# Kernel tuning notes

Hardware: AMD Instinct MI355X
Metric: run time of the kernel (lower is better)

## Reference

```python
import jax, jax.numpy as jnp
import numpy as np

N_NODES = 50000

def _gcn_layer(x, src, dst, W, b, n_nodes):
    # x: [N, F_in]; src/dst: [E+N] (self-loops already appended)
    h = x @ W  # [N, F_out]
    deg = jax.ops.segment_sum(jnp.ones_like(dst, dtype=h.dtype), dst, num_segments=n_nodes)
    dinv = jnp.where(deg > 0, jax.lax.rsqrt(deg), 0.0)  # deg^{-1/2}
    norm = dinv[src] * dinv[dst]  # [E+N]
    msg = h[src] * norm[:, None]  # gather + scale
    out = jax.ops.segment_sum(msg, dst, num_segments=n_nodes)  # scatter-add
    return out + b

def setup_inputs() -> dict:
    key = jax.random.key(0)
    k1, k2, k3, k4 = jax.random.split(key, 4)
    d = 128
    E = 800000
    x = jax.random.normal(k1, (N_NODES, d), dtype=jnp.float32)
    edge_index = jax.random.randint(k2, (2, E), 0, N_NODES, dtype=jnp.int64)
    W1 = jax.random.normal(k3, (d, d), dtype=jnp.float32) / np.sqrt(d)
    b1 = jnp.zeros((d,), dtype=jnp.float32)
    W2 = jax.random.normal(k4, (d, d), dtype=jnp.float32) / np.sqrt(d)
    b2 = jnp.zeros((d,), dtype=jnp.float32)
    return {"x": x, "edge_index": edge_index, "W1": W1, "b1": b1, "W2": W2, "b2": b2}

def reference(x, edge_index, W1, b1, W2, b2):
    n = x.shape[0]
    loops = jnp.arange(n, dtype=edge_index.dtype)
    src = jnp.concatenate([edge_index[0], loops])  # add self-loops
    dst = jnp.concatenate([edge_index[1], loops])
    h = _gcn_layer(x, src, dst, W1, b1, n)
    h = jax.nn.relu(h)
    z = _gcn_layer(h, src, dst, W2, b2, n)
    return z
```

## Files before the change

### kernel.cpp

```cpp
#include <hip/hip_runtime.h>
#include <hip/hip_fp16.h>

#define NF 128
#define NP 8192
#define KC 32

typedef _Float16 half8 __attribute__((ext_vector_type(8)));
typedef float    floatx4 __attribute__((ext_vector_type(4)));

__global__ __launch_bounds__(256) void prep_k(
    const float* __restrict__ W1, const float* __restrict__ W2,
    __half* __restrict__ WT1, __half* __restrict__ WT2)
{
    int idx = blockIdx.x * 256 + threadIdx.x;
    const float* W = (idx < 16384) ? W1 : W2;
    __half* WT     = (idx < 16384) ? WT1 : WT2;
    int j = idx & 16383;
    int nn = j & 127, k = j >> 7;
    WT[nn * NF + k] = __float2half(W[k * NF + nn]);
}

__global__ __launch_bounds__(512) void count2_k(
    const int* __restrict__ dst, int* __restrict__ pcnt, int E, int N, int Ec)
{
    __shared__ int lcnt[NP];
    const int p = blockIdx.x & 7, c = blockIdx.x >> 3;
    const int Np = (N + 7) >> 3;
    const int lo = p * Np, hi = min(lo + Np, N);
    const int sz = hi - lo;
    for (int i = threadIdx.x; i < sz; i += 512) lcnt[i] = 0;
    __syncthreads();

    const int e0 = c * Ec, e1 = min(e0 + Ec, E);
    for (int e = e0 + (int)threadIdx.x * 4; e + 3 < e1; e += 512 * 4) {
        int4 d = *(const int4*)(dst + e);
        if (d.x >= lo && d.x < hi) atomicAdd(&lcnt[d.x - lo], 1);
        if (d.y >= lo && d.y < hi) atomicAdd(&lcnt[d.y - lo], 1);
        if (d.z >= lo && d.z < hi) atomicAdd(&lcnt[d.z - lo], 1);
        if (d.w >= lo && d.w < hi) atomicAdd(&lcnt[d.w - lo], 1);
    }
    int rem0 = e0 + ((e1 - e0) & ~3);
    for (int e = rem0 + (int)threadIdx.x; e < e1; e += 512) {
        int d = dst[e];
        if (d >= lo && d < hi) atomicAdd(&lcnt[d - lo], 1);
    }
    __syncthreads();
    for (int i = threadIdx.x; i < sz; i += 512)
        pcnt[(size_t)c * N + lo + i] = lcnt[i];
}

__global__ __launch_bounds__(256) void pscan2_k(
    int* __restrict__ pcnt, float* __restrict__ dinv,
    int* __restrict__ rowptr, int* __restrict__ blocksum, int n, int N)
{
    __shared__ int sm[256];
    int tid = threadIdx.x;
    int bin = blockIdx.x * 256 + tid;
    int total = 0;
    if (bin < n) {
        #pragma unroll 4
        for (int c = 0; c < KC; c++) {
            size_t o = (size_t)c * N + bin;
            int v = pcnt[o];
            pcnt[o] = total;
            total += v;
        }
        dinv[bin] = rsqrtf((float)total + 1.0f);
    }
    sm[tid] = total;
    __syncthreads();
    #pragma unroll
    for (int d = 1; d < 256; d <<= 1) {
        int t = (tid >= d) ? sm[tid - d] : 0;
        __syncthreads();
        sm[tid] += t;
        __syncthreads();
    }
    if (bin < n) rowptr[bin] = sm[tid] - total;
    if (tid == 255) blocksum[blockIdx.x] = sm[255];
}

__global__ __launch_bounds__(256) void add_off2(
    int* __restrict__ rowptr, const int* __restrict__ blocksum, int n, int E, int nb)
{
    __shared__ int sm[256];
    int tid = threadIdx.x;
    sm[tid] = (tid < nb && tid < (int)blockIdx.x) ? blocksum[tid] : 0;
    __syncthreads();
    #pragma unroll
    for (int d = 128; d > 0; d >>= 1) {
        if (tid < d) sm[tid] += sm[tid + d];
        __syncthreads();
    }
    int offv = sm[0];
    int i = blockIdx.x * 256 + tid;
    if (i < n) rowptr[i] += offv;
    if (blockIdx.x == 0 && tid == 0) rowptr[n] = E;
}

__global__ __launch_bounds__(512) void fill2_k(
    const int* __restrict__ src, const int* __restrict__ dst,
    const int* __restrict__ rowptr, const int* __restrict__ coff,
    int* __restrict__ csr, int E, int N, int Ec)
{
    __shared__ int lcur[NP];
    const int p = blockIdx.x & 7, c = blockIdx.x >> 3;
    const int Np = (N + 7) >> 3;
    const int lo = p * Np, hi = min(lo + Np, N);
    const int sz = hi - lo;
    for (int i = threadIdx.x; i < sz; i += 512)
        lcur[i] = rowptr[lo + i] + coff[(size_t)c * N + lo + i];
    __syncthreads();

    const int e0 = c * Ec, e1 = min(e0 + Ec, E);
    for (int e = e0 + (int)threadIdx.x * 4; e + 3 < e1; e += 512 * 4) {
        int4 d = *(const int4*)(dst + e);
        int4 s = *(const int4*)(src + e);
        if (d.x >= lo && d.x < hi) csr[atomicAdd(&lcur[d.x - lo], 1)] = s.x;
        if (d.y >= lo && d.y < hi) csr[atomicAdd(&lcur[d.y - lo], 1)] = s.y;
        if (d.z >= lo && d.z < hi) csr[atomicAdd(&lcur[d.z - lo], 1)] = s.z;
        if (d.w >= lo && d.w < hi) csr[atomicAdd(&lcur[d.w - lo], 1)] = s.w;
    }
    int rem0 = e0 + ((e1 - e0) & ~3);
    for (int e = rem0 + (int)threadIdx.x; e < e1; e += 512) {
        int d = dst[e];
        if (d >= lo && d < hi) csr[atomicAdd(&lcur[d - lo], 1)] = src[e];
    }
}


template<bool F32IN>
__device__ __forceinline__ void gemm_body(
    const void* __restrict__ Xv, const __half* __restrict__ WT,
    const float* __restrict__ dinv, __half* __restrict__ out, int M, int bid)
{
    __shared__ __half wlds[128][136];
    const int tid = threadIdx.x;

    {
        int r = tid >> 1;
        int c0 = (tid & 1) * 64;
        const half8* s = (const half8*)(WT + (size_t)r * NF + c0);
        half8* d = (half8*)&wlds[r][c0];
        #pragma unroll
        for (int j = 0; j < 8; j++) d[j] = s[j];
    }
    __syncthreads();

    const int wave = tid >> 6, lane = tid & 63;
    const int quad = lane >> 4, l15 = lane & 15;
    const int rowA = bid * 64 + wave * 16 + l15;
    const int rowc = (rowA < M) ? rowA : (M - 1);

    half8 afr[4];
    if (F32IN) {
        const float* X = (const float*)Xv;
        #pragma unroll
        for (int kc = 0; kc < 4; kc++) {
            const floatx4* p = (const floatx4*)(X + (size_t)rowc * NF + kc * 32 + quad * 8);
            floatx4 u = p[0], v = p[1];
            half8 a;
            a[0] = (_Float16)u[0]; a[1] = (_Float16)u[1];
            a[2] = (_Float16)u[2]; a[3] = (_Float16)u[3];
            a[4] = (_Float16)v[0]; a[5] = (_Float16)v[1];
            a[6] = (_Float16)v[2]; a[7] = (_Float16)v[3];
            afr[kc] = a;
        }
    } else {
        const __half* X = (const __half*)Xv;
        #pragma unroll
        for (int kc = 0; kc < 4; kc++)
            afr[kc] = *(const half8*)(X + (size_t)rowc * NF + kc * 32 + quad * 8);
    }

    floatx4 acc[8];
    #pragma unroll
    for (int ct = 0; ct < 8; ct++) { floatx4 z = {0.f, 0.f, 0.f, 0.f}; acc[ct] = z; }

    #pragma unroll
    for (int kc = 0; kc < 4; kc++) {
        #pragma unroll
        for (int ct = 0; ct < 8; ct++) {
            half8 b = *(const half8*)&wlds[ct * 16 + l15][kc * 32 + quad * 8];
            acc[ct] = __builtin_amdgcn_mfma_f32_16x16x32_f16(afr[kc], b, acc[ct], 0, 0, 0);
        }
    }

    const int orow0 = bid * 64 + wave * 16 + quad * 4;
    #pragma unroll
    for (int r = 0; r < 4; r++) {
        int orow = orow0 + r;
        if (orow < M) {
            float s = dinv[orow];
            #pragma unroll
            for (int ct = 0; ct < 8; ct++)
                out[(size_t)orow * NF + ct * 16 + l15] = __float2half(acc[ct][r] * s);
        }
    }
}

__global__ __launch_bounds__(256) void gemm1_k(
    const float* __restrict__ X, const __half* __restrict__ WT,
    const float* __restrict__ dinv, __half* __restrict__ H, int M)
{
    gemm_body<true>(X, WT, dinv, H, M, blockIdx.x);
}

__global__ __launch_bounds__(256) void gemm2_k(
    const __half* __restrict__ A, const __half* __restrict__ WT,
    const float* __restrict__ dinv, __half* __restrict__ H, int M)
{
    gemm_body<false>(A, WT, dinv, H, M, blockIdx.x);
}


__global__ __launch_bounds__(256) void agg_k(
    const __half2* __restrict__ hs, const int* __restrict__ rowptr,
    const int* __restrict__ csr, const float* __restrict__ dinv,
    const float* __restrict__ bias, __half2* __restrict__ outh,
    float* __restrict__ outf, int n)
{
    int wave = threadIdx.x >> 6;
    int lane = threadIdx.x & 63;
    int node = blockIdx.x * 4 + wave;
    if (node >= n) return;

    const int HS = NF / 2;
    float2 acc = __half22float2(hs[(size_t)node * HS + lane]);

    int base = rowptr[node];
    int cnt  = rowptr[node + 1] - base;

    for (int off = 0; off < cnt; off += 64) {
        int m = min(64, cnt - off);
        int idx = 0;
        if (lane < m) idx = __builtin_nontemporal_load(&csr[base + off + lane]);
        int j = 0;
        for (; j + 15 < m; j += 16) {
            int s[16];
            __half2 v[16];
            #pragma unroll
            for (int t = 0; t < 16; t++) s[t] = __shfl(idx, j + t, 64);
            #pragma unroll
            for (int t = 0; t < 16; t++) v[t] = hs[(size_t)s[t] * HS + lane];
            #pragma unroll
            for (int t = 0; t < 16; t++) {
                float2 f = __half22float2(v[t]);
                acc.x += f.x; acc.y += f.y;
            }
        }
        for (; j + 3 < m; j += 4) {
            int s0 = __shfl(idx, j, 64);
            int s1 = __shfl(idx, j + 1, 64);
            int s2 = __shfl(idx, j + 2, 64);
            int s3 = __shfl(idx, j + 3, 64);
            __half2 v0 = hs[(size_t)s0 * HS + lane];
            __half2 v1 = hs[(size_t)s1 * HS + lane];
            __half2 v2 = hs[(size_t)s2 * HS + lane];
            __half2 v3 = hs[(size_t)s3 * HS + lane];
            float2 f0 = __half22float2(v0), f1 = __half22float2(v1);
            float2 f2 = __half22float2(v2), f3 = __half22float2(v3);
            acc.x += (f0.x + f1.x) + (f2.x + f3.x);
            acc.y += (f0.y + f1.y) + (f2.y + f3.y);
        }
        for (; j < m; j++) {
            int s0 = __shfl(idx, j, 64);
            float2 f0 = __half22float2(hs[(size_t)s0 * HS + lane]);
            acc.x += f0.x; acc.y += f0.y;
        }
    }

    float s = dinv[node];
    float ox = s * acc.x + bias[2 * lane];
    float oy = s * acc.y + bias[2 * lane + 1];
    if (outh) {
        ox = fmaxf(ox, 0.f); oy = fmaxf(oy, 0.f);
        outh[(size_t)node * HS + lane] = __floats2half2_rn(ox, oy);
    } else {
        ((float2*)(outf + (size_t)node * NF))[lane] = make_float2(ox, oy);
    }
}


extern "C" void kernel_launch(void* const* d_in, const int* in_sizes, int n_in,
                              void* d_out, int out_size, void* d_ws, size_t ws_size,
                              hipStream_t stream) {
    const float* x  = (const float*)d_in[0];
    const int*   ei = (const int*)d_in[1];
    const float* W1 = (const float*)d_in[2];
    const float* b1 = (const float*)d_in[3];
    const float* W2 = (const float*)d_in[4];
    const float* b2 = (const float*)d_in[5];
    float* out = (float*)d_out;

    const int N = in_sizes[0] / NF;
    const int E = in_sizes[1] / 2;
    const int* src = ei;
    const int* dst = ei + E;

    char* ws = (char*)d_ws;
    size_t off = 0;
    auto alloc = [&](size_t bytes) {
        void* p = ws + off;
        off += bytes;
        off = (off + 63) & ~(size_t)63;
        return p;
    };
    int*    pcnt   = (int*)alloc((size_t)KC * N * 4);
    int*    rowptr = (int*)alloc((size_t)(N + 1) * 4);
    int*    csr    = (int*)alloc((size_t)E * 4);
    float*  dinv   = (float*)alloc((size_t)N * 4);
    int*    bsum   = (int*)alloc((size_t)256 * 4);
    __half* WT1    = (__half*)alloc((size_t)NF * NF * 2);
    __half* WT2    = (__half*)alloc((size_t)NF * NF * 2);
    __half* H16    = (__half*)alloc((size_t)N * NF * 2);
    __half* A16    = (__half*)alloc((size_t)N * NF * 2);

    int nb = (N + 255) / 256;
    int Ec = (((E + KC - 1) / KC) + 3) & ~3;
    int gb = (N + 63) / 64;
    int ab = (N + 3) / 4;

    prep_k<<<128, 256, 0, stream>>>(W1, W2, WT1, WT2);
    count2_k<<<KC * 8, 512, 0, stream>>>(dst, pcnt, E, N, Ec);
    pscan2_k<<<nb, 256, 0, stream>>>(pcnt, dinv, rowptr, bsum, N, N);
    add_off2<<<nb, 256, 0, stream>>>(rowptr, bsum, N, E, nb);
    fill2_k<<<KC * 8, 512, 0, stream>>>(src, dst, rowptr, pcnt, csr, E, N, Ec);
    gemm1_k<<<gb, 256, 0, stream>>>(x, WT1, dinv, H16, N);
    agg_k<<<ab, 256, 0, stream>>>((const __half2*)H16, rowptr, csr, dinv, b1,
                                  (__half2*)A16, nullptr, N);
    gemm2_k<<<gb, 256, 0, stream>>>(A16, WT2, dinv, H16, N);
    agg_k<<<ab, 256, 0, stream>>>((const __half2*)H16, rowptr, csr, dinv, b2,
                                  nullptr, out, N);
}
```

Measured before the change: 217.3 us.

## Fuse weight prep into scan kernel, repartition CSR build, unify agg tail

Folds the weight transpose/convert kernel into extra blocks of the prefix-scan kernel, removing one launch. The count and fill passes now use 4 node partitions with 64 edge chunks instead of 8 partitions with 32 chunks, so each block holds a larger shared-memory slab (12544 ints) and each edge is scanned by fewer blocks. The aggregation tail replaces the 4-wide and scalar remainder loops with one predicated 8-wide loop that issues more loads at once. The tradeoffs are more shared memory per block (lower occupancy), a per-block pcnt that is twice as large for the scan to walk, and some redundant clamped gathers in the tail.

```diff
diff --git a/kernel.cpp b/kernel.cpp
--- a/kernel.cpp
+++ b/kernel.cpp
@@ -2,30 +2,18 @@
 #include <hip/hip_fp16.h>
 
 #define NF 128
-#define NP 8192
-#define KC 32
+#define KC 64
+#define NPART 4
 
 typedef _Float16 half8 __attribute__((ext_vector_type(8)));
 typedef float    floatx4 __attribute__((ext_vector_type(4)));
 
-__global__ __launch_bounds__(256) void prep_k(
-    const float* __restrict__ W1, const float* __restrict__ W2,
-    __half* __restrict__ WT1, __half* __restrict__ WT2)
-{
-    int idx = blockIdx.x * 256 + threadIdx.x;
-    const float* W = (idx < 16384) ? W1 : W2;
-    __half* WT     = (idx < 16384) ? WT1 : WT2;
-    int j = idx & 16383;
-    int nn = j & 127, k = j >> 7;
-    WT[nn * NF + k] = __float2half(W[k * NF + nn]);
-}
-
 __global__ __launch_bounds__(512) void count2_k(
     const int* __restrict__ dst, int* __restrict__ pcnt, int E, int N, int Ec)
 {
-    __shared__ int lcnt[NP];
-    const int p = blockIdx.x & 7, c = blockIdx.x >> 3;
-    const int Np = (N + 7) >> 3;
+    __shared__ int lcnt[12544];
+    const int p = blockIdx.x & 3, c = blockIdx.x >> 2;
+    const int Np = (N + 3) >> 2;
     const int lo = p * Np, hi = min(lo + Np, N);
     const int sz = hi - lo;
     for (int i = threadIdx.x; i < sz; i += 512) lcnt[i] = 0;
@@ -51,8 +39,19 @@
 
 __global__ __launch_bounds__(256) void pscan2_k(
     int* __restrict__ pcnt, float* __restrict__ dinv,
-    int* __restrict__ rowptr, int* __restrict__ blocksum, int n, int N)
-{
+    int* __restrict__ rowptr, int* __restrict__ blocksum, int n, int N, int nb,
+    const float* __restrict__ W1, const float* __restrict__ W2,
+    __half* __restrict__ WT1, __half* __restrict__ WT2)
+{
+    if ((int)blockIdx.x >= nb) {
+        int idx = ((int)blockIdx.x - nb) * 256 + threadIdx.x;
+        const float* W = (idx < 16384) ? W1 : W2;
+        __half* WT     = (idx < 16384) ? WT1 : WT2;
+        int j = idx & 16383;
+        int nn = j & 127, k = j >> 7;
+        WT[nn * NF + k] = __float2half(W[k * NF + nn]);
+        return;
+    }
     __shared__ int sm[256];
     int tid = threadIdx.x;
     int bin = blockIdx.x * 256 + tid;
@@ -103,9 +102,9 @@
     const int* __restrict__ rowptr, const int* __restrict__ coff,
     int* __restrict__ csr, int E, int N, int Ec)
 {
-    __shared__ int lcur[NP];
-    const int p = blockIdx.x & 7, c = blockIdx.x >> 3;
-    const int Np = (N + 7) >> 3;
+    __shared__ int lcur[12544];
+    const int p = blockIdx.x & 3, c = blockIdx.x >> 2;
+    const int Np = (N + 3) >> 2;
     const int lo = p * Np, hi = min(lo + Np, N);
     const int sz = hi - lo;
     for (int i = threadIdx.x; i < sz; i += 512)
@@ -249,24 +248,20 @@
                 acc.x += f.x; acc.y += f.y;
             }
         }
-        for (; j + 3 < m; j += 4) {
-            int s0 = __shfl(idx, j, 64);
-            int s1 = __shfl(idx, j + 1, 64);
-            int s2 = __shfl(idx, j + 2, 64);
-            int s3 = __shfl(idx, j + 3, 64);
-            __half2 v0 = hs[(size_t)s0 * HS + lane];
-            __half2 v1 = hs[(size_t)s1 * HS + lane];
-            __half2 v2 = hs[(size_t)s2 * HS + lane];
-            __half2 v3 = hs[(size_t)s3 * HS + lane];
-            float2 f0 = __half22float2(v0), f1 = __half22float2(v1);
-            float2 f2 = __half22float2(v2), f3 = __half22float2(v3);
-            acc.x += (f0.x + f1.x) + (f2.x + f3.x);
-            acc.y += (f0.y + f1.y) + (f2.y + f3.y);
-        }
-        for (; j < m; j++) {
-            int s0 = __shfl(idx, j, 64);
-            float2 f0 = __half22float2(hs[(size_t)s0 * HS + lane]);
-            acc.x += f0.x; acc.y += f0.y;
+        for (; j < m; j += 8) {
+            int s[8];
+            __half2 v[8];
+            #pragma unroll
+            for (int t = 0; t < 8; t++) s[t] = __shfl(idx, min(j + t, m - 1), 64);
+            #pragma unroll
+            for (int t = 0; t < 8; t++) v[t] = hs[(size_t)s[t] * HS + lane];
+            #pragma unroll
+            for (int t = 0; t < 8; t++) {
+                if (j + t < m) {
+                    float2 f = __half22float2(v[t]);
+                    acc.x += f.x; acc.y += f.y;
+                }
+            }
         }
     }
 
@@ -321,11 +316,11 @@
     int gb = (N + 63) / 64;
     int ab = (N + 3) / 4;
 
-    prep_k<<<128, 256, 0, stream>>>(W1, W2, WT1, WT2);
-    count2_k<<<KC * 8, 512, 0, stream>>>(dst, pcnt, E, N, Ec);
-    pscan2_k<<<nb, 256, 0, stream>>>(pcnt, dinv, rowptr, bsum, N, N);
+    count2_k<<<KC * NPART, 512, 0, stream>>>(dst, pcnt, E, N, Ec);
+    pscan2_k<<<nb + 128, 256, 0, stream>>>(pcnt, dinv, rowptr, bsum, N, N, nb,
+                                           W1, W2, WT1, WT2);
     add_off2<<<nb, 256, 0, stream>>>(rowptr, bsum, N, E, nb);
-    fill2_k<<<KC * 8, 512, 0, stream>>>(src, dst, rowptr, pcnt, csr, E, N, Ec);
+    fill2_k<<<KC * NPART, 512, 0, stream>>>(src, dst, rowptr, pcnt, csr, E, N, Ec);
     gemm1_k<<<gb, 256, 0, stream>>>(x, WT1, dinv, H16, N);
     agg_k<<<ab, 256, 0, stream>>>((const __half2*)H16, rowptr, csr, dinv, b1,
                                   (__half2*)A16, nullptr, N);
```

Measured after the change: 216.3 us. Within noise of the previous version (-0.5%).
